# Kernel tuning notes

Hardware: AMD Instinct MI355X
Metric: run time of the kernel (lower is better)

## Reference

```python
import jax, jax.numpy as jnp
import numpy as np

B, N, C, NSAMPLE = 4, 1024, 512, 32
RADIUS, HMIN, HMAX = 0.05, -0.02, 0.04
EPS = 1e-5


def setup_inputs() -> dict:
    key = jax.random.key(0)
    ks = jax.random.split(key, 6)
    # points in a ~20cm cube so the 5cm cylinder actually captures neighbors
    seed_xyz_graspable = jax.random.uniform(ks[0], (B, N, 3), jnp.float32) * 0.2
    seed_features_graspable = jax.random.normal(ks[1], (B, C, N), jnp.float32)
    rot_raw = jax.random.normal(ks[2], (B, N, 3, 3), jnp.float32)
    vp_rot, _ = jnp.linalg.qr(rot_raw)  # proper-ish per-seed view rotations
    W1 = jax.random.normal(ks[3], (512, 3 + C), jnp.float32) / np.float32(np.sqrt(3 + C))
    g1 = jnp.ones((512,), jnp.float32)
    b1 = jnp.zeros((512,), jnp.float32)
    W2 = jax.random.normal(ks[4], (512, 512), jnp.float32) / np.float32(np.sqrt(512))
    g2 = jnp.ones((512,), jnp.float32)
    b2 = jnp.zeros((512,), jnp.float32)
    return dict(seed_xyz_graspable=seed_xyz_graspable,
                seed_features_graspable=seed_features_graspable,
                vp_rot=vp_rot, W1=W1, g1=g1, b1=b1, W2=W2, g2=g2, b2=b2)


def _cylinder_query(xyz, rot):
    # offsets d[b,m,n] = xyz[b,n] - query[b,m], rotated into the cylinder frame (d @ R)
    d = xyz[:, None, :, :] - xyz[:, :, None, :]                 # (B,M,N,3)
    r = jnp.einsum('bmnd,bmde->bmne', d, rot)                   # (B,M,N,3)
    mask = (r[..., 1] ** 2 + r[..., 2] ** 2 < RADIUS ** 2) \
         & (r[..., 0] > HMIN) & (r[..., 0] < HMAX)              # (B,M,N)
    # first NSAMPLE valid indices; pad with the first valid index (CUDA kernel semantics)
    cand = jnp.where(mask, jnp.arange(N, dtype=jnp.int32)[None, None, :], N)
    idx = jnp.sort(cand, axis=-1)[..., :NSAMPLE]                # (B,M,S)
    idx = jnp.where(idx == N, idx[..., :1], idx)
    return idx


def _bn_relu(x, g, b):
    # training-mode BatchNorm2d over (B, M, S) per output channel; x: (B,O,M,S)
    mean = jnp.mean(x, axis=(0, 2, 3), keepdims=True)
    var = jnp.var(x, axis=(0, 2, 3), keepdims=True)
    xn = (x - mean) * jax.lax.rsqrt(var + EPS)
    return jax.nn.relu(xn * g[None, :, None, None] + b[None, :, None, None])


def reference(seed_xyz_graspable, seed_features_graspable, vp_rot, W1, g1, b1, W2, g2, b2):
    xyz = seed_xyz_graspable                                    # (B,N,3)
    idx = _cylinder_query(xyz, vp_rot)                          # (B,M,S) int32
    # gather neighbor coordinates and center/rotate/normalize
    grouped_xyz = jnp.take_along_axis(xyz[:, None], idx[..., None], axis=2)   # (B,M,S,3)
    local = grouped_xyz - xyz[:, :, None, :]
    local = jnp.einsum('bmsd,bmde->bmse', local, vp_rot) / RADIUS             # normalize_xyz
    # gather neighbor features
    feats = jnp.swapaxes(seed_features_graspable, 1, 2)                       # (B,N,C)
    gfeat = jnp.take_along_axis(feats[:, None], idx[..., None], axis=2)       # (B,M,S,C)
    x = jnp.concatenate([local, gfeat], axis=-1)                              # (B,M,S,3+C)
    # SharedMLP: 1x1 conv (no bias) + BN + ReLU, twice; channels-first layout (B,O,M,S)
    h = _bn_relu(jnp.einsum('bmsc,oc->boms', x, W1), g1, b1)
    h = _bn_relu(jnp.einsum('boms,po->bpms', h, W2), g2, b2)
    # max-pool over the nsample axis -> (B,512,M)
    return jnp.max(h, axis=-1)
```

## Files before the change

### kernel.cpp

```cpp
#include <hip/hip_runtime.h>
#include <hip/hip_bf16.h>
#include <stdint.h>

#define BATCH 4
#define NPTS  1024
#define CIN   512
#define NS    32
#define P_TOT (BATCH*NPTS*NS)
#define CO    512
#define RADIUS_F 0.05f
#define HMIN_F  (-0.02f)
#define HMAX_F  (0.04f)

typedef __attribute__((ext_vector_type(8))) short short8;
typedef __attribute__((ext_vector_type(4))) float f32x4;

__device__ __forceinline__ unsigned short f2bf(float f) {
  unsigned int x = __float_as_uint(f);
  x = x + 0x7fffu + ((x >> 16) & 1u);
  return (unsigned short)(x >> 16);
}
__device__ __forceinline__ float bf2f(unsigned short u) {
  return __uint_as_float(((unsigned int)u) << 16);
}
__device__ __forceinline__ unsigned int cvtpk(float lo, float hi) {
  unsigned int r;
  asm("v_cvt_pk_bf16_f32 %0, %1, %2" : "=v"(r) : "v"(lo), "v"(hi));
  return r;
}
__device__ __forceinline__ void load_lds16(const void* g, void* l) {
  __builtin_amdgcn_global_load_lds((const __attribute__((address_space(1))) void*)g,
                                   (__attribute__((address_space(3))) void*)l, 16, 0, 0);
}

__global__ void cyl_query_kernel(const float* __restrict__ xyz,
                                 const float* __restrict__ rot,
                                 int* __restrict__ idxout,
                                 float* __restrict__ lxyz) {
  int bm = blockIdx.x;
  int b = bm >> 10;
  int lane = threadIdx.x;
  const float* ctr = xyz + (size_t)bm * 3;
  float cx = ctr[0], cy = ctr[1], cz = ctr[2];
  const float* R = rot + (size_t)bm * 9;
  float r00=R[0],r01=R[1],r02=R[2],r10=R[3],r11=R[4],r12=R[5],r20=R[6],r21=R[7],r22=R[8];
  __shared__ int sidx[32];
  int taken = 0;
  for (int base = 0; base < NPTS && taken < NS; base += 64) {
    int n = base + lane;
    const float* p = xyz + ((size_t)b * NPTS + n) * 3;
    float dx = p[0]-cx, dy = p[1]-cy, dz = p[2]-cz;
    float rx = dx*r00 + dy*r10 + dz*r20;
    float ry = dx*r01 + dy*r11 + dz*r21;
    float rz = dx*r02 + dy*r12 + dz*r22;
    bool ok = (ry*ry + rz*rz < RADIUS_F*RADIUS_F) && (rx > HMIN_F) && (rx < HMAX_F);
    unsigned long long bal = __ballot(ok);
    if (ok) {
      int slot = taken + __popcll(bal & ((1ull << lane) - 1ull));
      if (slot < NS) sidx[slot] = n;
    }
    taken += __popcll(bal);
  }
  __syncthreads();
  int filled = taken < NS ? taken : NS;
  if (lane < NS) {
    int nsel = (lane < filled) ? sidx[lane] : sidx[0];
    size_t pp = (size_t)bm * NS + lane;
    idxout[pp] = nsel;
    const float* pn = xyz + ((size_t)b * NPTS + nsel) * 3;
    float dx = pn[0]-cx, dy = pn[1]-cy, dz = pn[2]-cz;
    const float inv = 1.0f / RADIUS_F;
    float rx = (dx*r00 + dy*r10 + dz*r20) * inv;
    float ry = (dx*r01 + dy*r11 + dz*r21) * inv;
    float rz = (dx*r02 + dy*r12 + dz*r22) * inv;
    float* lw = lxyz + pp * 3;
    lw[0] = rx; lw[1] = ry; lw[2] = rz;
  }
}

__global__ void transpose_feats(const float* __restrict__ feats,
                                unsigned short* __restrict__ featsT) {
  __shared__ float tile[64][65];
  int b = blockIdx.z, cb = blockIdx.y, nb = blockIdx.x;
  int t = threadIdx.x, tr = t >> 6, tc = t & 63;
  #pragma unroll
  for (int j = 0; j < 16; ++j) {
    int c = cb*64 + j*4 + tr;
    tile[j*4+tr][tc] = feats[((size_t)b*CIN + c)*NPTS + nb*64 + tc];
  }
  __syncthreads();
  #pragma unroll
  for (int j = 0; j < 16; ++j) {
    int n = nb*64 + j*4 + tr;
    featsT[((size_t)b*NPTS + n)*CIN + cb*64 + tc] = f2bf(tile[tc][j*4+tr]);
  }
}

__global__ void build_w1(const float* __restrict__ W1,
                         unsigned short* __restrict__ w1f,
                         float* __restrict__ w1l) {
  int i = blockIdx.x*256 + threadIdx.x;
  if (i < 512*512) {
    int o = i >> 9, k = i & 511;
    w1f[i] = f2bf(W1[o*515 + 3 + k]);
  }
  if (i < 512*3) {
    w1l[i] = W1[(i/3)*515 + (i%3)];
  }
}
__global__ void build_w2(const float* __restrict__ W2, unsigned short* __restrict__ w2b) {
  int i = blockIdx.x*256 + threadIdx.x;
  if (i < CO*CIN) w2b[i] = f2bf(W2[i]);
}

__global__ __launch_bounds__(256) void scatter_kernel(
    const int* __restrict__ idx, const float* __restrict__ lxyz,
    float* __restrict__ L4, float* __restrict__ GM) {
  int i = blockIdx.x*256 + threadIdx.x;
  int b = i >> 15;
  int n = idx[i];
  const float* lw = lxyz + (size_t)i*3;
  float lx = lw[0], ly = lw[1], lz = lw[2];
  float* dst = L4 + (((size_t)b << 10) + n)*4;
  atomicAdd(dst+0, lx); atomicAdd(dst+1, ly);
  atomicAdd(dst+2, lz); atomicAdd(dst+3, 1.0f);
  float m[9] = {lx, ly, lz, lx*lx, lx*ly, lx*lz, ly*ly, ly*lz, lz*lz};
  #pragma unroll
  for (int d = 1; d < 64; d <<= 1)
    #pragma unroll
    for (int e = 0; e < 9; ++e) m[e] += __shfl_xor(m[e], d);
  __shared__ float mred[9];
  if (threadIdx.x < 9) mred[threadIdx.x] = 0.f;
  __syncthreads();
  if ((threadIdx.x & 63) == 0)
    #pragma unroll
    for (int e = 0; e < 9; ++e) atomicAdd(&mred[e], m[e]);
  __syncthreads();
  if (threadIdx.x < 9) atomicAdd(&GM[threadIdx.x], mred[threadIdx.x]);
}

__global__ __launch_bounds__(256) void gemm1u_kernel(
    const unsigned short* __restrict__ A,
    const unsigned short* __restrict__ Bw,
    float* __restrict__ C)
{
  __shared__ unsigned short As[128*32];
  __shared__ unsigned short Bs[128*32];
  int bx = blockIdx.x;
  int ob = bx & 3;
  size_t p0 = (size_t)(bx >> 2) * 128;
  int o0 = ob * 128;
  int t = threadIdx.x;
  int w = t >> 6, lane = t & 63;
  int wr = w >> 1, wc = w & 1;
  int l15 = lane & 15, l4 = lane >> 4;
  f32x4 acc[4][4];
  f32x4 zf = {0.f, 0.f, 0.f, 0.f};
  #pragma unroll
  for (int mi = 0; mi < 4; ++mi)
    #pragma unroll
    for (int ni = 0; ni < 4; ++ni) acc[mi][ni] = zf;

  int c0 = 2*w;
  int srow = lane >> 2;
  int scole = (lane & 3) * 8;

  const unsigned short* abase[2];
  const unsigned short* bbase[2];
  #pragma unroll
  for (int cc = 0; cc < 2; ++cc) {
    int row = 16*(c0+cc) + srow;
    abase[cc] = A + (p0 + row)*(size_t)512 + scole;
    bbase[cc] = Bw + (size_t)(o0 + row)*512 + scole;
  }

  for (int k0 = 0; k0 < 512; k0 += 32) {
    #pragma unroll
    for (int cc = 0; cc < 2; ++cc) {
      int c = c0 + cc;
      load_lds16(abase[cc] + k0, (char*)As + c*1024);
      load_lds16(bbase[cc] + k0, (char*)Bs + c*1024);
    }
    __syncthreads();
    short8 af[4], bfr[4];
    #pragma unroll
    for (int mi = 0; mi < 4; ++mi)
      af[mi] = *(const short8*)(As + (wr*64 + mi*16 + l15)*32 + l4*8);
    #pragma unroll
    for (int ni = 0; ni < 4; ++ni)
      bfr[ni] = *(const short8*)(Bs + (wc*64 + ni*16 + l15)*32 + l4*8);
    #pragma unroll
    for (int mi = 0; mi < 4; ++mi)
      #pragma unroll
      for (int ni = 0; ni < 4; ++ni)
        acc[mi][ni] = __builtin_amdgcn_mfma_f32_16x16x32_bf16(af[mi], bfr[ni], acc[mi][ni], 0, 0, 0);
    __syncthreads();
  }
  #pragma unroll
  for (int mi = 0; mi < 4; ++mi)
    #pragma unroll
    for (int ni = 0; ni < 4; ++ni)
      #pragma unroll
      for (int j = 0; j < 4; ++j) {
        size_t p = p0 + wr*64 + mi*16 + l4*4 + j;
        int o = o0 + wc*64 + ni*16 + l15;
        C[p*512 + o] = acc[mi][ni][j];
      }
}

__global__ __launch_bounds__(256) void stats1_kernel(
    const float* __restrict__ h1u, const float* __restrict__ L4,
    const float* __restrict__ w1l, float* __restrict__ sums) {
  int t = threadIdx.x;
  int c2 = t*2;
  int u0 = blockIdx.x * 16;
  float w0a = w1l[c2*3],     w1a = w1l[c2*3+1],     w2a = w1l[c2*3+2];
  float w0b = w1l[(c2+1)*3], w1b = w1l[(c2+1)*3+1], w2b = w1l[(c2+1)*3+2];
  float s0=0.f, s1=0.f, q0=0.f, q1=0.f;
  #pragma unroll 4
  for (int j = 0; j < 16; ++j) {
    int u = u0 + j;
    float4 Lc = *(const float4*)(L4 + (size_t)u*4);
    float2 h = *(const float2*)(h1u + (size_t)u*512 + c2);
    float lwa = Lc.x*w0a + Lc.y*w1a + Lc.z*w2a;
    float lwb = Lc.x*w0b + Lc.y*w1b + Lc.z*w2b;
    s0 += Lc.w*h.x;  q0 += Lc.w*h.x*h.x + 2.f*h.x*lwa;
    s1 += Lc.w*h.y;  q1 += Lc.w*h.y*h.y + 2.f*h.y*lwb;
  }
  atomicAdd(&sums[c2],       s0);
  atomicAdd(&sums[c2+1],     s1);
  atomicAdd(&sums[512+c2],   q0);
  atomicAdd(&sums[512+c2+1], q1);
}

__global__ void finalize1_kernel(const float* __restrict__ sums,
                                 const float* __restrict__ GM,
                                 const float* __restrict__ w1l,
                                 const float* __restrict__ g,
                                 const float* __restrict__ bia,
                                 float* __restrict__ ss,
                                 float* __restrict__ w1ls) {
  int c = blockIdx.x*256 + threadIdx.x;
  if (c >= 512) return;
  float w0 = w1l[c*3], w1 = w1l[c*3+1], w2 = w1l[c*3+2];
  float S = sums[c] + w0*GM[0] + w1*GM[1] + w2*GM[2];
  float Q = sums[512+c] + w0*w0*GM[3] + 2.f*w0*w1*GM[4] + 2.f*w0*w2*GM[5]
                        + w1*w1*GM[6] + 2.f*w1*w2*GM[7] + w2*w2*GM[8];
  const float invN = 1.f / (float)P_TOT;
  float mean = S * invN;
  float var  = Q * invN - mean*mean;
  float sc = g[c] * rsqrtf(var + 1e-5f);
  ss[c] = sc;
  ss[512+c] = bia[c] - mean*sc;
  w1ls[c]        = sc * w0;
  w1ls[512 + c]  = sc * w1;
  w1ls[1024 + c] = sc * w2;
}

__global__ __launch_bounds__(256) void fold_kernel(float* __restrict__ h1u,
                                                   const float* __restrict__ ss) {
  size_t i = ((size_t)blockIdx.x*256 + threadIdx.x) * 4;
  int c = (int)(i & 511);
  float4 v = *(float4*)(h1u + i);
  float4 sc = *(const float4*)(ss + c);
  float4 sh = *(const float4*)(ss + 512 + c);
  v.x = fmaf(v.x, sc.x, sh.x);
  v.y = fmaf(v.y, sc.y, sh.y);
  v.z = fmaf(v.z, sc.z, sh.z);
  v.w = fmaf(v.w, sc.w, sh.w);
  *(float4*)(h1u + i) = v;
}

__global__ void finalize_kernel(const float* __restrict__ sums,
                                const float* __restrict__ g,
                                const float* __restrict__ bia,
                                float* __restrict__ ss) {
  int c = blockIdx.x*256 + threadIdx.x;
  if (c >= 512) return;
  const float invN = 1.f / (float)P_TOT;
  float mean = sums[c] * invN;
  float var  = sums[512+c] * invN - mean*mean;
  float sc = g[c] * rsqrtf(var + 1e-5f);
  ss[c] = sc;
  ss[512+c] = bia[c] - mean*sc;
}

__global__ __launch_bounds__(512) void gemm2_kernel(
    const float* __restrict__ h1u,
    const int* __restrict__ idx,
    const float* __restrict__ lxyz,
    const float* __restrict__ w1ls,
    const unsigned short* __restrict__ Bw,
    float* __restrict__ sums,
    float* __restrict__ pmax,
    float* __restrict__ pmin)
{
  __shared__ unsigned short As[128*32];
  __shared__ unsigned short Bs[256*32];
  __shared__ float wl[1536];
  int bx = blockIdx.x;
  int ob = bx & 1;
  size_t p0 = (size_t)(bx >> 1) * 128;
  int o0 = ob * 256;
  int t = threadIdx.x;
  int w = t >> 6, lane = t & 63;
  int wr = w >> 2;
  int wc = w & 3;
  int l15 = lane & 15, l4 = lane >> 4;
  f32x4 acc[4][4];
  f32x4 zf = {0.f, 0.f, 0.f, 0.f};
  #pragma unroll
  for (int mi = 0; mi < 4; ++mi)
    #pragma unroll
    for (int ni = 0; ni < 4; ++ni) acc[mi][ni] = zf;

  int sl = (lane & 3) ^ ((lane >> 3) & 3);
  int scole = (lane & 3) * 8;
  int cA = (l4 ^ ((l15 >> 1) & 3)) * 8;

  wl[t] = w1ls[t]; wl[512 + t] = w1ls[512 + t]; wl[1024 + t] = w1ls[1024 + t];

  int arow = 16*w + (lane >> 2);
  int awoff = arow*64 + sl*16;
  const float* hptr;
  float lxr, lyr, lzr;
  {
    size_t p = p0 + arow;
    int b = (int)(p >> 15);
    int n = idx[p];
    hptr = h1u + (((size_t)b << 10) + n)*512 + scole;
    const float* lwp = lxyz + p*3;
    lxr = lwp[0]; lyr = lwp[1]; lzr = lwp[2];
  }
  const unsigned short* bptr[2];
  #pragma unroll
  for (int cc = 0; cc < 2; ++cc) {
    int brow = 16*(2*w + cc) + (lane >> 2);
    bptr[cc] = Bw + (size_t)(o0 + brow)*CIN + sl*8;
  }

  float4 hv0 = *(const float4*)(hptr);
  float4 hv1 = *(const float4*)(hptr + 4);
  __syncthreads();

  for (int k0 = 0; k0 < CIN; k0 += 32) {
    #pragma unroll
    for (int cc = 0; cc < 2; ++cc)
      load_lds16(bptr[cc] + k0, (char*)Bs + (2*w + cc)*1024);
    int ch0 = k0 + scole;
    float4 xa = *(const float4*)(wl + ch0);
    float4 xb = *(const float4*)(wl + ch0 + 4);
    float4 ya = *(const float4*)(wl + 512 + ch0);
    float4 yb = *(const float4*)(wl + 512 + ch0 + 4);
    float4 za = *(const float4*)(wl + 1024 + ch0);
    float4 zb = *(const float4*)(wl + 1024 + ch0 + 4);
    float w0[8] = {xa.x,xa.y,xa.z,xa.w,xb.x,xb.y,xb.z,xb.w};
    float w1[8] = {ya.x,ya.y,ya.z,ya.w,yb.x,yb.y,yb.z,yb.w};
    float w2[8] = {za.x,za.y,za.z,za.w,zb.x,zb.y,zb.z,zb.w};
    {
      float fv[8] = {hv0.x, hv0.y, hv0.z, hv0.w, hv1.x, hv1.y, hv1.z, hv1.w};
      float gv[8];
      #pragma unroll
      for (int e = 0; e < 8; ++e)
        gv[e] = fmaxf(fv[e] + lxr*w0[e] + lyr*w1[e] + lzr*w2[e], 0.f);
      unsigned int rv[4];
      #pragma unroll
      for (int j = 0; j < 4; ++j) rv[j] = cvtpk(gv[2*j], gv[2*j+1]);
      *(uint4*)((char*)As + awoff) = make_uint4(rv[0], rv[1], rv[2], rv[3]);
    }
    if (k0 + 32 < CIN) {
      hv0 = *(const float4*)(hptr + k0 + 32);
      hv1 = *(const float4*)(hptr + k0 + 36);
    }
    __syncthreads();
    short8 af[4], bfr[4];
    #pragma unroll
    for (int mi = 0; mi < 4; ++mi)
      af[mi] = *(const short8*)(As + (wr*64 + mi*16 + l15)*32 + cA);
    #pragma unroll
    for (int ni = 0; ni < 4; ++ni)
      bfr[ni] = *(const short8*)(Bs + (wc*64 + ni*16 + l15)*32 + cA);
    #pragma unroll
    for (int mi = 0; mi < 4; ++mi)
      #pragma unroll
      for (int ni = 0; ni < 4; ++ni)
        acc[mi][ni] = __builtin_amdgcn_mfma_f32_16x16x32_bf16(af[mi], bfr[ni], acc[mi][ni], 0, 0, 0);
    __syncthreads();
  }

  #pragma unroll
  for (int ni = 0; ni < 4; ++ni) {
    float s = 0.f, q = 0.f;
    #pragma unroll
    for (int mi = 0; mi < 4; ++mi)
      #pragma unroll
      for (int j = 0; j < 4; ++j) { float v = acc[mi][ni][j]; s += v; q += v*v; }
    s += __shfl_xor(s, 16); q += __shfl_xor(q, 16);
    s += __shfl_xor(s, 32); q += __shfl_xor(q, 32);
    if (l4 == 0) {
      int c = o0 + wc*64 + ni*16 + l15;
      atomicAdd(&sums[c], s);
      atomicAdd(&sums[512 + c], q);
    }
  }
  #pragma unroll
  for (int ni = 0; ni < 4; ++ni) {
    #pragma unroll
    for (int h = 0; h < 2; ++h) {
      float mx = -3.4e38f, mn = 3.4e38f;
      #pragma unroll
      for (int mi = 2*h; mi < 2*h + 2; ++mi)
        #pragma unroll
        for (int j = 0; j < 4; ++j) {
          float v = acc[mi][ni][j];
          mx = fmaxf(mx, v); mn = fminf(mn, v);
        }
      mx = fmaxf(mx, __shfl_xor(mx, 16)); mn = fminf(mn, __shfl_xor(mn, 16));
      mx = fmaxf(mx, __shfl_xor(mx, 32)); mn = fminf(mn, __shfl_xor(mn, 32));
      if (l4 == 0) {
        size_t bm = (p0 >> 5) + 2*wr + h;
        int o = o0 + wc*64 + ni*16 + l15;
        pmax[bm*512 + o] = mx;
        pmin[bm*512 + o] = mn;
      }
    }
  }
}

__global__ void final_transpose(const float* __restrict__ pmax,
                                const float* __restrict__ pmin,
                                const float* __restrict__ ss,
                                float* __restrict__ out) {
  __shared__ float tile[64][65];
  int b = blockIdx.z, ob = blockIdx.y, mb = blockIdx.x;
  int t = threadIdx.x, tr = t >> 6, tc = t & 63;
  #pragma unroll
  for (int j = 0; j < 16; ++j) {
    int m = mb*64 + j*4 + tr;
    int o = ob*64 + tc;
    float sc = ss[o], sh = ss[512+o];
    size_t pi = (((size_t)b << 10) + m)*512 + o;
    float v = (sc >= 0.f) ? pmax[pi] : pmin[pi];
    tile[j*4+tr][tc] = fmaxf(fmaf(v, sc, sh), 0.f);
  }
  __syncthreads();
  #pragma unroll
  for (int j = 0; j < 16; ++j) {
    int o = ob*64 + j*4 + tr;
    out[((size_t)b*512 + o)*1024 + mb*64 + tc] = tile[tc][j*4+tr];
  }
}

extern "C" void kernel_launch(void* const* d_in, const int* in_sizes, int n_in,
                              void* d_out, int out_size, void* d_ws, size_t ws_size,
                              hipStream_t stream) {
  const float* xyz   = (const float*)d_in[0];
  const float* feats = (const float*)d_in[1];
  const float* rot   = (const float*)d_in[2];
  const float* W1    = (const float*)d_in[3];
  const float* g1    = (const float*)d_in[4];
  const float* b1    = (const float*)d_in[5];
  const float* W2    = (const float*)d_in[6];
  const float* g2    = (const float*)d_in[7];
  const float* b2    = (const float*)d_in[8];
  float* out = (float*)d_out;
  char* wsb = (char*)d_ws;

  const size_t OFF_IDX    = 0;
  const size_t OFF_LXYZ   = OFF_IDX    + (size_t)P_TOT*4;
  const size_t OFF_FEATST = OFF_LXYZ   + (size_t)P_TOT*3*4;
  const size_t OFF_W1F    = OFF_FEATST + (size_t)BATCH*NPTS*CIN*2;
  const size_t OFF_W1L    = OFF_W1F    + (size_t)CO*512*2;
  const size_t OFF_W1LS   = OFF_W1L    + 8192;
  const size_t OFF_W2B    = OFF_W1LS   + 8192;
  const size_t OFF_STATS  = OFF_W2B    + (size_t)CO*CIN*2;
  const size_t OFF_L4     = OFF_STATS  + 16384;
  const size_t OFF_GM     = OFF_L4     + 65536;
  const size_t OFF_H1U    = OFF_GM     + 4096;
  const size_t OFF_PMAX   = OFF_H1U    + (size_t)BATCH*NPTS*CO*4;
  const size_t OFF_PMIN   = OFF_PMAX   + (size_t)BATCH*NPTS*CO*4;
  const size_t WS_NEED    = OFF_PMIN   + (size_t)BATCH*NPTS*CO*4;

  if (ws_size < WS_NEED) return;

  int* idx             = (int*)(wsb + OFF_IDX);
  float* lxyz          = (float*)(wsb + OFF_LXYZ);
  unsigned short* fT   = (unsigned short*)(wsb + OFF_FEATST);
  unsigned short* w1f  = (unsigned short*)(wsb + OFF_W1F);
  float* w1l           = (float*)(wsb + OFF_W1L);
  float* w1ls          = (float*)(wsb + OFF_W1LS);
  unsigned short* w2b  = (unsigned short*)(wsb + OFF_W2B);
  float* stats         = (float*)(wsb + OFF_STATS);
  float* sums1 = stats;
  float* ss1   = stats + 1024;
  float* sums2 = stats + 2048;
  float* ss2   = stats + 3072;
  float* L4            = (float*)(wsb + OFF_L4);
  float* GM            = (float*)(wsb + OFF_GM);
  float* h1u           = (float*)(wsb + OFF_H1U);
  float* pmax          = (float*)(wsb + OFF_PMAX);
  float* pmin          = (float*)(wsb + OFF_PMIN);

  hipMemsetAsync(stats, 0, 16384 + 65536 + 4096, stream);

  transpose_feats<<<dim3(NPTS/64, CIN/64, BATCH), 256, 0, stream>>>(feats, fT);
  cyl_query_kernel<<<BATCH*NPTS, 64, 0, stream>>>(xyz, rot, idx, lxyz);
  build_w1<<<(512*512 + 255)/256, 256, 0, stream>>>(W1, w1f, w1l);
  build_w2<<<(CO*CIN + 255)/256, 256, 0, stream>>>(W2, w2b);

  scatter_kernel<<<P_TOT/256, 256, 0, stream>>>(idx, lxyz, L4, GM);
  gemm1u_kernel<<<(BATCH*NPTS/128)*4, 256, 0, stream>>>(fT, w1f, h1u);
  stats1_kernel<<<256, 256, 0, stream>>>(h1u, L4, w1l, sums1);
  finalize1_kernel<<<2, 256, 0, stream>>>(sums1, GM, w1l, g1, b1, ss1, w1ls);
  fold_kernel<<<(BATCH*NPTS*CO/4)/256, 256, 0, stream>>>(h1u, ss1);

  gemm2_kernel<<<(P_TOT/128)*2, 512, 0, stream>>>(h1u, idx, lxyz, w1ls, w2b,
                                                  sums2, pmax, pmin);
  finalize_kernel<<<2, 256, 0, stream>>>(sums2, g2, b2, ss2);

  final_transpose<<<dim3(NPTS/64, CO/64, BATCH), 256, 0, stream>>>(pmax, pmin, ss2, out);
}
```

Baseline: 216.2 us.

## Widen gemm2 tile to all 512 output channels with 1024-thread blocks

The second GEMM now has each block cover all 512 output channels for its 128 rows, using 16 waves instead of 8, rather than splitting outputs across two blocks. This halves the number of times the gathered h1 rows are loaded and the BN/ReLU prologue is recomputed per point. Each thread now stages 4 channels instead of 8, using a new swizzled LDS write. The two weight-conversion kernels are also merged into one launch. The larger block and doubled B tile in LDS may reduce occupancy and add barrier cost.

```diff
diff --git a/kernel.cpp b/kernel.cpp
--- a/kernel.cpp
+++ b/kernel.cpp
@@ -96,21 +96,20 @@
   }
 }
 
-__global__ void build_w1(const float* __restrict__ W1,
-                         unsigned short* __restrict__ w1f,
-                         float* __restrict__ w1l) {
+__global__ void build_weights(const float* __restrict__ W1,
+                              const float* __restrict__ W2,
+                              unsigned short* __restrict__ w1f,
+                              float* __restrict__ w1l,
+                              unsigned short* __restrict__ w2b) {
   int i = blockIdx.x*256 + threadIdx.x;
   if (i < 512*512) {
     int o = i >> 9, k = i & 511;
     w1f[i] = f2bf(W1[o*515 + 3 + k]);
+    w2b[i] = f2bf(W2[i]);
   }
   if (i < 512*3) {
     w1l[i] = W1[(i/3)*515 + (i%3)];
   }
-}
-__global__ void build_w2(const float* __restrict__ W2, unsigned short* __restrict__ w2b) {
-  int i = blockIdx.x*256 + threadIdx.x;
-  if (i < CO*CIN) w2b[i] = f2bf(W2[i]);
 }
 
 __global__ __launch_bounds__(256) void scatter_kernel(
@@ -285,7 +284,7 @@
   ss[512+c] = bia[c] - mean*sc;
 }
 
-__global__ __launch_bounds__(512) void gemm2_kernel(
+__global__ __launch_bounds__(1024) void gemm2_kernel(
     const float* __restrict__ h1u,
     const int* __restrict__ idx,
     const float* __restrict__ lxyz,
@@ -296,16 +295,14 @@
     float* __restrict__ pmin)
 {
   __shared__ unsigned short As[128*32];
-  __shared__ unsigned short Bs[256*32];
+  __shared__ unsigned short Bs[512*32];
   __shared__ float wl[1536];
   int bx = blockIdx.x;
-  int ob = bx & 1;
-  size_t p0 = (size_t)(bx >> 1) * 128;
-  int o0 = ob * 256;
+  size_t p0 = (size_t)bx * 128;
   int t = threadIdx.x;
   int w = t >> 6, lane = t & 63;
-  int wr = w >> 2;
-  int wc = w & 3;
+  int wr = w >> 3;
+  int wc = w & 7;
   int l15 = lane & 15, l4 = lane >> 4;
   f32x4 acc[4][4];
   f32x4 zf = {0.f, 0.f, 0.f, 0.f};
@@ -315,20 +312,22 @@
     for (int ni = 0; ni < 4; ++ni) acc[mi][ni] = zf;
 
   int sl = (lane & 3) ^ ((lane >> 3) & 3);
-  int scole = (lane & 3) * 8;
   int cA = (l4 ^ ((l15 >> 1) & 3)) * 8;
 
-  wl[t] = w1ls[t]; wl[512 + t] = w1ls[512 + t]; wl[1024 + t] = w1ls[1024 + t];
-
-  int arow = 16*w + (lane >> 2);
-  int awoff = arow*64 + sl*16;
+  wl[t] = w1ls[t];
+  if (t < 512) wl[1024 + t] = w1ls[1024 + t];
+
+  int arow = 8*w + (lane >> 3);
+  int c4 = (lane & 7) * 4;
+  int s16 = (lane & 7) >> 1;
+  int awoff = arow*64 + ((s16 ^ ((arow >> 1) & 3)) << 4) + (lane & 1)*8;
   const float* hptr;
   float lxr, lyr, lzr;
   {
     size_t p = p0 + arow;
     int b = (int)(p >> 15);
     int n = idx[p];
-    hptr = h1u + (((size_t)b << 10) + n)*512 + scole;
+    hptr = h1u + (((size_t)b << 10) + n)*512 + c4;
     const float* lwp = lxyz + p*3;
     lxr = lwp[0]; lyr = lwp[1]; lzr = lwp[2];
   }
@@ -336,42 +335,28 @@
   #pragma unroll
   for (int cc = 0; cc < 2; ++cc) {
     int brow = 16*(2*w + cc) + (lane >> 2);
-    bptr[cc] = Bw + (size_t)(o0 + brow)*CIN + sl*8;
-  }
-
-  float4 hv0 = *(const float4*)(hptr);
-  float4 hv1 = *(const float4*)(hptr + 4);
+    bptr[cc] = Bw + (size_t)brow*CIN + sl*8;
+  }
+
+  float4 hv = *(const float4*)(hptr);
   __syncthreads();
 
   for (int k0 = 0; k0 < CIN; k0 += 32) {
     #pragma unroll
     for (int cc = 0; cc < 2; ++cc)
       load_lds16(bptr[cc] + k0, (char*)Bs + (2*w + cc)*1024);
-    int ch0 = k0 + scole;
-    float4 xa = *(const float4*)(wl + ch0);
-    float4 xb = *(const float4*)(wl + ch0 + 4);
-    float4 ya = *(const float4*)(wl + 512 + ch0);
-    float4 yb = *(const float4*)(wl + 512 + ch0 + 4);
-    float4 za = *(const float4*)(wl + 1024 + ch0);
-    float4 zb = *(const float4*)(wl + 1024 + ch0 + 4);
-    float w0[8] = {xa.x,xa.y,xa.z,xa.w,xb.x,xb.y,xb.z,xb.w};
-    float w1[8] = {ya.x,ya.y,ya.z,ya.w,yb.x,yb.y,yb.z,yb.w};
-    float w2[8] = {za.x,za.y,za.z,za.w,zb.x,zb.y,zb.z,zb.w};
+    float4 xa = *(const float4*)(wl + k0 + c4);
+    float4 ya = *(const float4*)(wl + 512 + k0 + c4);
+    float4 za = *(const float4*)(wl + 1024 + k0 + c4);
     {
-      float fv[8] = {hv0.x, hv0.y, hv0.z, hv0.w, hv1.x, hv1.y, hv1.z, hv1.w};
-      float gv[8];
-      #pragma unroll
-      for (int e = 0; e < 8; ++e)
-        gv[e] = fmaxf(fv[e] + lxr*w0[e] + lyr*w1[e] + lzr*w2[e], 0.f);
-      unsigned int rv[4];
-      #pragma unroll
-      for (int j = 0; j < 4; ++j) rv[j] = cvtpk(gv[2*j], gv[2*j+1]);
-      *(uint4*)((char*)As + awoff) = make_uint4(rv[0], rv[1], rv[2], rv[3]);
+      float g0 = fmaxf(hv.x + lxr*xa.x + lyr*ya.x + lzr*za.x, 0.f);
+      float g1 = fmaxf(hv.y + lxr*xa.y + lyr*ya.y + lzr*za.y, 0.f);
+      float g2 = fmaxf(hv.z + lxr*xa.z + lyr*ya.z + lzr*za.z, 0.f);
+      float g3 = fmaxf(hv.w + lxr*xa.w + lyr*ya.w + lzr*za.w, 0.f);
+      uint2 rv = make_uint2(cvtpk(g0, g1), cvtpk(g2, g3));
+      *(uint2*)((char*)As + awoff) = rv;
     }
-    if (k0 + 32 < CIN) {
-      hv0 = *(const float4*)(hptr + k0 + 32);
-      hv1 = *(const float4*)(hptr + k0 + 36);
-    }
+    if (k0 + 32 < CIN) hv = *(const float4*)(hptr + k0 + 32);
     __syncthreads();
     short8 af[4], bfr[4];
     #pragma unroll
@@ -398,7 +383,7 @@
     s += __shfl_xor(s, 16); q += __shfl_xor(q, 16);
     s += __shfl_xor(s, 32); q += __shfl_xor(q, 32);
     if (l4 == 0) {
-      int c = o0 + wc*64 + ni*16 + l15;
+      int c = wc*64 + ni*16 + l15;
       atomicAdd(&sums[c], s);
       atomicAdd(&sums[512 + c], q);
     }
@@ -419,7 +404,7 @@
       mx = fmaxf(mx, __shfl_xor(mx, 32)); mn = fminf(mn, __shfl_xor(mn, 32));
       if (l4 == 0) {
         size_t bm = (p0 >> 5) + 2*wr + h;
-        int o = o0 + wc*64 + ni*16 + l15;
+        int o = wc*64 + ni*16 + l15;
         pmax[bm*512 + o] = mx;
         pmin[bm*512 + o] = mn;
       }
@@ -505,8 +490,7 @@
 
   transpose_feats<<<dim3(NPTS/64, CIN/64, BATCH), 256, 0, stream>>>(feats, fT);
   cyl_query_kernel<<<BATCH*NPTS, 64, 0, stream>>>(xyz, rot, idx, lxyz);
-  build_w1<<<(512*512 + 255)/256, 256, 0, stream>>>(W1, w1f, w1l);
-  build_w2<<<(CO*CIN + 255)/256, 256, 0, stream>>>(W2, w2b);
+  build_weights<<<(512*512 + 255)/256, 256, 0, stream>>>(W1, W2, w1f, w1l, w2b);
 
   scatter_kernel<<<P_TOT/256, 256, 0, stream>>>(idx, lxyz, L4, GM);
   gemm1u_kernel<<<(BATCH*NPTS/128)*4, 256, 0, stream>>>(fT, w1f, h1u);
@@ -514,8 +498,8 @@
   finalize1_kernel<<<2, 256, 0, stream>>>(sums1, GM, w1l, g1, b1, ss1, w1ls);
   fold_kernel<<<(BATCH*NPTS*CO/4)/256, 256, 0, stream>>>(h1u, ss1);
 
-  gemm2_kernel<<<(P_TOT/128)*2, 512, 0, stream>>>(h1u, idx, lxyz, w1ls, w2b,
-                                                  sums2, pmax, pmin);
+  gemm2_kernel<<<P_TOT/128, 1024, 0, stream>>>(h1u, idx, lxyz, w1ls, w2b,
+                                               sums2, pmax, pmin);
   finalize_kernel<<<2, 256, 0, stream>>>(sums2, g2, b2, ss2);
 
   final_transpose<<<dim3(NPTS/64, CO/64, BATCH), 256, 0, stream>>>(pmax, pmin, ss2, out);
```

Result: slower. 225.9 us (+4.5%).

## Fuse BN stats into GEMM1, fold BN affine into GEMM2, merge small kernels

Applied to the files above, without the earlier changes.

Computes layer-1 BN partial sums in the GEMM1 epilogue from register accumulators instead of re-reading h1u in a separate stats kernel. Applies the layer-1 scale/shift inside GEMM2's A-tile load rather than in a separate in-place fold pass over h1u. It also merges the two weight-conversion kernels and folds the layer-2 finalize into the final transpose. This removes several full passes over an 8MB buffer and a few launches, at the cost of extra per-element FMA work in GEMM2 and more atomics in the GEMM1 epilogue.

```diff
diff --git a/kernel.cpp b/kernel.cpp
--- a/kernel.cpp
+++ b/kernel.cpp
@@ -96,21 +96,20 @@
   }
 }
 
-__global__ void build_w1(const float* __restrict__ W1,
-                         unsigned short* __restrict__ w1f,
-                         float* __restrict__ w1l) {
+__global__ void build_weights(const float* __restrict__ W1,
+                              const float* __restrict__ W2,
+                              unsigned short* __restrict__ w1f,
+                              float* __restrict__ w1l,
+                              unsigned short* __restrict__ w2b) {
   int i = blockIdx.x*256 + threadIdx.x;
   if (i < 512*512) {
     int o = i >> 9, k = i & 511;
     w1f[i] = f2bf(W1[o*515 + 3 + k]);
+    w2b[i] = f2bf(W2[i]);
   }
   if (i < 512*3) {
     w1l[i] = W1[(i/3)*515 + (i%3)];
   }
-}
-__global__ void build_w2(const float* __restrict__ W2, unsigned short* __restrict__ w2b) {
-  int i = blockIdx.x*256 + threadIdx.x;
-  if (i < CO*CIN) w2b[i] = f2bf(W2[i]);
 }
 
 __global__ __launch_bounds__(256) void scatter_kernel(
@@ -142,7 +141,10 @@
 __global__ __launch_bounds__(256) void gemm1u_kernel(
     const unsigned short* __restrict__ A,
     const unsigned short* __restrict__ Bw,
-    float* __restrict__ C)
+    float* __restrict__ C,
+    const float* __restrict__ L4,
+    const float* __restrict__ w1l,
+    float* __restrict__ sums)
 {
   __shared__ unsigned short As[128*32];
   __shared__ unsigned short Bs[128*32];
@@ -206,31 +208,29 @@
         int o = o0 + wc*64 + ni*16 + l15;
         C[p*512 + o] = acc[mi][ni][j];
       }
-}
-
-__global__ __launch_bounds__(256) void stats1_kernel(
-    const float* __restrict__ h1u, const float* __restrict__ L4,
-    const float* __restrict__ w1l, float* __restrict__ sums) {
-  int t = threadIdx.x;
-  int c2 = t*2;
-  int u0 = blockIdx.x * 16;
-  float w0a = w1l[c2*3],     w1a = w1l[c2*3+1],     w2a = w1l[c2*3+2];
-  float w0b = w1l[(c2+1)*3], w1b = w1l[(c2+1)*3+1], w2b = w1l[(c2+1)*3+2];
-  float s0=0.f, s1=0.f, q0=0.f, q1=0.f;
-  #pragma unroll 4
-  for (int j = 0; j < 16; ++j) {
-    int u = u0 + j;
-    float4 Lc = *(const float4*)(L4 + (size_t)u*4);
-    float2 h = *(const float2*)(h1u + (size_t)u*512 + c2);
-    float lwa = Lc.x*w0a + Lc.y*w1a + Lc.z*w2a;
-    float lwb = Lc.x*w0b + Lc.y*w1b + Lc.z*w2b;
-    s0 += Lc.w*h.x;  q0 += Lc.w*h.x*h.x + 2.f*h.x*lwa;
-    s1 += Lc.w*h.y;  q1 += Lc.w*h.y*h.y + 2.f*h.y*lwb;
-  }
-  atomicAdd(&sums[c2],       s0);
-  atomicAdd(&sums[c2+1],     s1);
-  atomicAdd(&sums[512+c2],   q0);
-  atomicAdd(&sums[512+c2+1], q1);
+  #pragma unroll
+  for (int ni = 0; ni < 4; ++ni) {
+    int c = o0 + wc*64 + ni*16 + l15;
+    float wa = w1l[c*3], wb = w1l[c*3+1], wcc = w1l[c*3+2];
+    float s = 0.f, q = 0.f;
+    #pragma unroll
+    for (int mi = 0; mi < 4; ++mi)
+      #pragma unroll
+      for (int j = 0; j < 4; ++j) {
+        size_t p = p0 + wr*64 + mi*16 + l4*4 + j;
+        float4 L = *(const float4*)(L4 + p*4);
+        float h = acc[mi][ni][j];
+        float lw = L.x*wa + L.y*wb + L.z*wcc;
+        s += L.w*h;
+        q += L.w*h*h + 2.f*h*lw;
+      }
+    s += __shfl_xor(s, 16); q += __shfl_xor(q, 16);
+    s += __shfl_xor(s, 32); q += __shfl_xor(q, 32);
+    if (l4 == 0) {
+      atomicAdd(&sums[c], s);
+      atomicAdd(&sums[512 + c], q);
+    }
+  }
 }
 
 __global__ void finalize1_kernel(const float* __restrict__ sums,
@@ -257,39 +257,12 @@
   w1ls[1024 + c] = sc * w2;
 }
 
-__global__ __launch_bounds__(256) void fold_kernel(float* __restrict__ h1u,
-                                                   const float* __restrict__ ss) {
-  size_t i = ((size_t)blockIdx.x*256 + threadIdx.x) * 4;
-  int c = (int)(i & 511);
-  float4 v = *(float4*)(h1u + i);
-  float4 sc = *(const float4*)(ss + c);
-  float4 sh = *(const float4*)(ss + 512 + c);
-  v.x = fmaf(v.x, sc.x, sh.x);
-  v.y = fmaf(v.y, sc.y, sh.y);
-  v.z = fmaf(v.z, sc.z, sh.z);
-  v.w = fmaf(v.w, sc.w, sh.w);
-  *(float4*)(h1u + i) = v;
-}
-
-__global__ void finalize_kernel(const float* __restrict__ sums,
-                                const float* __restrict__ g,
-                                const float* __restrict__ bia,
-                                float* __restrict__ ss) {
-  int c = blockIdx.x*256 + threadIdx.x;
-  if (c >= 512) return;
-  const float invN = 1.f / (float)P_TOT;
-  float mean = sums[c] * invN;
-  float var  = sums[512+c] * invN - mean*mean;
-  float sc = g[c] * rsqrtf(var + 1e-5f);
-  ss[c] = sc;
-  ss[512+c] = bia[c] - mean*sc;
-}
-
 __global__ __launch_bounds__(512) void gemm2_kernel(
     const float* __restrict__ h1u,
     const int* __restrict__ idx,
     const float* __restrict__ lxyz,
     const float* __restrict__ w1ls,
+    const float* __restrict__ ss,
     const unsigned short* __restrict__ Bw,
     float* __restrict__ sums,
     float* __restrict__ pmax,
@@ -298,6 +271,7 @@
   __shared__ unsigned short As[128*32];
   __shared__ unsigned short Bs[256*32];
   __shared__ float wl[1536];
+  __shared__ float ssl[1024];
   int bx = blockIdx.x;
   int ob = bx & 1;
   size_t p0 = (size_t)(bx >> 1) * 128;
@@ -319,6 +293,7 @@
   int cA = (l4 ^ ((l15 >> 1) & 3)) * 8;
 
   wl[t] = w1ls[t]; wl[512 + t] = w1ls[512 + t]; wl[1024 + t] = w1ls[1024 + t];
+  ssl[t] = ss[t]; ssl[512 + t] = ss[512 + t];
 
   int arow = 16*w + (lane >> 2);
   int awoff = arow*64 + sl*16;
@@ -354,15 +329,23 @@
     float4 yb = *(const float4*)(wl + 512 + ch0 + 4);
     float4 za = *(const float4*)(wl + 1024 + ch0);
     float4 zb = *(const float4*)(wl + 1024 + ch0 + 4);
+    float4 sA = *(const float4*)(ssl + ch0);
+    float4 sB = *(const float4*)(ssl + ch0 + 4);
+    float4 hA = *(const float4*)(ssl + 512 + ch0);
+    float4 hB = *(const float4*)(ssl + 512 + ch0 + 4);
     float w0[8] = {xa.x,xa.y,xa.z,xa.w,xb.x,xb.y,xb.z,xb.w};
     float w1[8] = {ya.x,ya.y,ya.z,ya.w,yb.x,yb.y,yb.z,yb.w};
     float w2[8] = {za.x,za.y,za.z,za.w,zb.x,zb.y,zb.z,zb.w};
+    float sc_[8] = {sA.x,sA.y,sA.z,sA.w,sB.x,sB.y,sB.z,sB.w};
+    float sh_[8] = {hA.x,hA.y,hA.z,hA.w,hB.x,hB.y,hB.z,hB.w};
     {
-      float fv[8] = {hv0.x, hv0.y, hv0.z, hv0.w, hv1.x, hv1.y, hv1.z, hv1.w};
+      float hvr[8] = {hv0.x, hv0.y, hv0.z, hv0.w, hv1.x, hv1.y, hv1.z, hv1.w};
       float gv[8];
       #pragma unroll
-      for (int e = 0; e < 8; ++e)
-        gv[e] = fmaxf(fv[e] + lxr*w0[e] + lyr*w1[e] + lzr*w2[e], 0.f);
+      for (int e = 0; e < 8; ++e) {
+        float fv = fmaf(hvr[e], sc_[e], sh_[e]);
+        gv[e] = fmaxf(fv + lxr*w0[e] + lyr*w1[e] + lzr*w2[e], 0.f);
+      }
       unsigned int rv[4];
       #pragma unroll
       for (int j = 0; j < 4; ++j) rv[j] = cvtpk(gv[2*j], gv[2*j+1]);
@@ -429,17 +412,29 @@
 
 __global__ void final_transpose(const float* __restrict__ pmax,
                                 const float* __restrict__ pmin,
-                                const float* __restrict__ ss,
+                                const float* __restrict__ sums,
+                                const float* __restrict__ g,
+                                const float* __restrict__ bia,
                                 float* __restrict__ out) {
   __shared__ float tile[64][65];
+  __shared__ float scl[64], shl[64];
   int b = blockIdx.z, ob = blockIdx.y, mb = blockIdx.x;
   int t = threadIdx.x, tr = t >> 6, tc = t & 63;
+  if (t < 64) {
+    int c = ob*64 + t;
+    const float invN = 1.f / (float)P_TOT;
+    float mean = sums[c] * invN;
+    float var  = sums[512+c] * invN - mean*mean;
+    float sc = g[c] * rsqrtf(var + 1e-5f);
+    scl[t] = sc;
+    shl[t] = bia[c] - mean*sc;
+  }
+  __syncthreads();
   #pragma unroll
   for (int j = 0; j < 16; ++j) {
     int m = mb*64 + j*4 + tr;
-    int o = ob*64 + tc;
-    float sc = ss[o], sh = ss[512+o];
-    size_t pi = (((size_t)b << 10) + m)*512 + o;
+    float sc = scl[tc], sh = shl[tc];
+    size_t pi = (((size_t)b << 10) + m)*512 + ob*64 + tc;
     float v = (sc >= 0.f) ? pmax[pi] : pmin[pi];
     tile[j*4+tr][tc] = fmaxf(fmaf(v, sc, sh), 0.f);
   }
@@ -494,7 +489,6 @@
   float* sums1 = stats;
   float* ss1   = stats + 1024;
   float* sums2 = stats + 2048;
-  float* ss2   = stats + 3072;
   float* L4            = (float*)(wsb + OFF_L4);
   float* GM            = (float*)(wsb + OFF_GM);
   float* h1u           = (float*)(wsb + OFF_H1U);
@@ -504,19 +498,16 @@
   hipMemsetAsync(stats, 0, 16384 + 65536 + 4096, stream);
 
   transpose_feats<<<dim3(NPTS/64, CIN/64, BATCH), 256, 0, stream>>>(feats, fT);
+  build_weights<<<(512*512 + 255)/256, 256, 0, stream>>>(W1, W2, w1f, w1l, w2b);
   cyl_query_kernel<<<BATCH*NPTS, 64, 0, stream>>>(xyz, rot, idx, lxyz);
-  build_w1<<<(512*512 + 255)/256, 256, 0, stream>>>(W1, w1f, w1l);
-  build_w2<<<(CO*CIN + 255)/256, 256, 0, stream>>>(W2, w2b);
-
   scatter_kernel<<<P_TOT/256, 256, 0, stream>>>(idx, lxyz, L4, GM);
-  gemm1u_kernel<<<(BATCH*NPTS/128)*4, 256, 0, stream>>>(fT, w1f, h1u);
-  stats1_kernel<<<256, 256, 0, stream>>>(h1u, L4, w1l, sums1);
+
+  gemm1u_kernel<<<(BATCH*NPTS/128)*4, 256, 0, stream>>>(fT, w1f, h1u, L4, w1l, sums1);
   finalize1_kernel<<<2, 256, 0, stream>>>(sums1, GM, w1l, g1, b1, ss1, w1ls);
-  fold_kernel<<<(BATCH*NPTS*CO/4)/256, 256, 0, stream>>>(h1u, ss1);
-
-  gemm2_kernel<<<(P_TOT/128)*2, 512, 0, stream>>>(h1u, idx, lxyz, w1ls, w2b,
+
+  gemm2_kernel<<<(P_TOT/128)*2, 512, 0, stream>>>(h1u, idx, lxyz, w1ls, ss1, w2b,
                                                   sums2, pmax, pmin);
-  finalize_kernel<<<2, 256, 0, stream>>>(sums2, g2, b2, ss2);
-
-  final_transpose<<<dim3(NPTS/64, CO/64, BATCH), 256, 0, stream>>>(pmax, pmin, ss2, out);
-}
+
+  final_transpose<<<dim3(NPTS/64, CO/64, BATCH), 256, 0, stream>>>(pmax, pmin,
+                                                                   sums2, g2, b2, out);
+}
```

Result: no change. 213.5 us (-1.2%).
